# Kernel optimization log

Measured on AMD Instinct MI355X. Metric: run time of the kernel, lower is better.

Reference implementation:

```python
import jax, jax.numpy as jnp
import numpy as np

N, T, D, H = 4, 2048, 1024, 16
DK = D // H

def setup_inputs() -> dict:
    key = jax.random.key(0)
    k1, k2, k3 = jax.random.split(key, 3)
    z = jax.random.normal(k1, (N, T, D), dtype=jnp.float32)
    Wqkv = jax.random.normal(k2, (D, 3 * D), dtype=jnp.float32) * 0.01
    Wout = jax.random.normal(k3, (D, D), dtype=jnp.float32) * 0.01
    return {"z": z, "Wqkv": Wqkv, "Wout": Wout}

def reference(z, Wqkv, Wout):
    n, t, d = z.shape
    scale = DK ** -0.5
    qkv = z @ Wqkv  # [N,T,3D]
    q, k, v = jnp.split(qkv, 3, axis=-1)
    # [N,T,D] -> [N,H,T,dk]
    q = q.reshape(n, t, H, DK).transpose(0, 2, 1, 3)
    k = k.reshape(n, t, H, DK).transpose(0, 2, 1, 3)
    v = v.reshape(n, t, H, DK).transpose(0, 2, 1, 3)
    attn = jnp.einsum('nhqd,nhkd->nhqk', q, k) * scale
    causal = jnp.tril(jnp.ones((t, t), dtype=bool))
    attn = jnp.where(causal, attn, -jnp.inf)
    attn = jax.nn.softmax(attn, axis=-1)
    out = jnp.einsum('nhqk,nhkd->nhqd', attn, v)  # [N,H,T,dk]
    out = out.transpose(0, 2, 1, 3).reshape(n, t, d)
    return out @ Wout
```

## Files before the change

kernel.cpp:

```cpp
#include <hip/hip_runtime.h>
#include <hip/hip_bf16.h>

typedef __bf16 bf16;
typedef __bf16 bf16x8 __attribute__((ext_vector_type(8)));
typedef float f32x4 __attribute__((ext_vector_type(4)));

#define N_B 4
#define T_S 2048
#define D_M 1024
#define H_N 16
#define D_K 64
#define D3 3072
#define NEG_BIG (-1e30f)
#define QSCALE 0.18033688011112042f

#if __has_builtin(__builtin_amdgcn_exp2f)
#define EXP2(x) __builtin_amdgcn_exp2f(x)
#else
#define EXP2(x) exp2f(x)
#endif

__device__ __forceinline__ void gload_lds16(const bf16* g, bf16* l) {
    __builtin_amdgcn_global_load_lds((const __attribute__((address_space(1))) void*)g,
                                     (__attribute__((address_space(3))) void*)l, 16, 0, 0);
}

__device__ __forceinline__ bool probe_fp32(const void* p) {
    const unsigned int* w = (const unsigned int*)p;
    int weird = 0;
#pragma unroll
    for (int i = 0; i < 16; ++i) {
        unsigned int v = w[i];
        unsigned int e = (v >> 7) & 0xFFu;
        if ((v & 0xFFFFu) != 0u && (e < 100u || e > 140u)) weird++;
    }
    return weird >= 4;
}

__global__ __launch_bounds__(256) void prep(const void* __restrict__ z, bf16* __restrict__ zb,
                                            const void* __restrict__ Wqkv, bf16* __restrict__ WqkvT,
                                            const void* __restrict__ Wout, bf16* __restrict__ WoutT) {
    __shared__ bf16 tile[32][33];
    const int b = blockIdx.x;
    const int t = threadIdx.x;

    if (b < 4096) {
        const int i = (b * 256 + t) * 8;
        if (probe_fp32(z)) {
            const float* zf = (const float*)z;
            float4 u0 = *(const float4*)(zf + i);
            float4 u1 = *(const float4*)(zf + i + 4);
            union { uint4 q; bf16 h[8]; } pk;
            pk.h[0] = (bf16)u0.x; pk.h[1] = (bf16)u0.y;
            pk.h[2] = (bf16)u0.z; pk.h[3] = (bf16)u0.w;
            pk.h[4] = (bf16)u1.x; pk.h[5] = (bf16)u1.y;
            pk.h[6] = (bf16)u1.z; pk.h[7] = (bf16)u1.w;
            *(uint4*)(zb + i) = pk.q;
        } else {
            *(uint4*)(zb + i) = ((const uint4*)z)[b * 256 + t];
        }
        return;
    }

    const void* in; bf16* out; int R, C, c0, r0;
    if (b < 7168) {
        int idx = b - 4096;
        in = Wqkv; out = WqkvT; R = 1024; C = 3072;
        c0 = (idx % 96) * 32; r0 = (idx / 96) * 32;
    } else {
        int idx = b - 7168;
        in = Wout; out = WoutT; R = 1024; C = 1024;
        c0 = (idx & 31) * 32; r0 = (idx >> 5) * 32;
    }
    const int tx = t & 31, ty = t >> 5;
    if (probe_fp32(in)) {
        const float* inf_ = (const float*)in;
        for (int i = 0; i < 4; ++i)
            tile[ty + i * 8][tx] = (bf16)inf_[(size_t)(r0 + ty + i * 8) * C + c0 + tx];
    } else {
        const bf16* inb = (const bf16*)in;
        for (int i = 0; i < 4; ++i)
            tile[ty + i * 8][tx] = inb[(size_t)(r0 + ty + i * 8) * C + c0 + tx];
    }
    __syncthreads();
    for (int i = 0; i < 4; ++i)
        out[(size_t)(c0 + ty + i * 8) * R + r0 + tx] = tile[tx][ty + i * 8];
}

__global__ __launch_bounds__(512, 2) void gemm256(const bf16* __restrict__ A,
                                                  const bf16* __restrict__ Bt,
                                                  void* __restrict__ C,
                                                  bf16* __restrict__ Kf,
                                                  bf16* __restrict__ Vf,
                                                  int M, int N, int K,
                                                  int modeC) {
    __shared__ bf16 As[3][256 * 64];
    __shared__ bf16 Bs[3][128 * 64];
    const int t = threadIdx.x;
    const int m0 = blockIdx.y * 256, n0 = blockIdx.x * 128;
    const int w = t >> 6, lane = t & 63, quad = lane >> 4, l15 = lane & 15;
    const int wr = (w >> 1) * 64, wc = (w & 1) * 64;
    const int sr = t >> 3;
    const int sg = ((t & 7) ^ (sr & 7)) * 8;
    const int xorL = (l15 & 7) * 8;

    const bf16* a0 = A + (size_t)(m0 + sr) * K + sg;
    const bf16* a1 = A + (size_t)(m0 + 64 + sr) * K + sg;
    const bf16* a2 = A + (size_t)(m0 + 128 + sr) * K + sg;
    const bf16* a3 = A + (size_t)(m0 + 192 + sr) * K + sg;
    const bf16* b0 = Bt + (size_t)(n0 + sr) * K + sg;
    const bf16* b1 = Bt + (size_t)(n0 + 64 + sr) * K + sg;
    const int ldsOff = w * 512;

    f32x4 acc[4][4];
    const f32x4 zero4 = {0.f, 0.f, 0.f, 0.f};
#pragma unroll
    for (int i = 0; i < 4; ++i)
#pragma unroll
        for (int j = 0; j < 4; ++j) acc[i][j] = zero4;

    const int nt = K >> 6;

    gload_lds16(a0, &As[0][0 * 4096 + ldsOff]);
    gload_lds16(a1, &As[0][1 * 4096 + ldsOff]);
    gload_lds16(a2, &As[0][2 * 4096 + ldsOff]);
    gload_lds16(a3, &As[0][3 * 4096 + ldsOff]);
    gload_lds16(b0, &Bs[0][0 * 4096 + ldsOff]);
    gload_lds16(b1, &Bs[0][1 * 4096 + ldsOff]);
    if (nt > 1) {
        gload_lds16(a0 + 64, &As[1][0 * 4096 + ldsOff]);
        gload_lds16(a1 + 64, &As[1][1 * 4096 + ldsOff]);
        gload_lds16(a2 + 64, &As[1][2 * 4096 + ldsOff]);
        gload_lds16(a3 + 64, &As[1][3 * 4096 + ldsOff]);
        gload_lds16(b0 + 64, &Bs[1][0 * 4096 + ldsOff]);
        gload_lds16(b1 + 64, &Bs[1][1 * 4096 + ldsOff]);
        asm volatile("s_waitcnt vmcnt(6)" ::: "memory");
    } else {
        asm volatile("s_waitcnt vmcnt(0)" ::: "memory");
    }
    __builtin_amdgcn_sched_barrier(0);
    __builtin_amdgcn_s_barrier();
    __builtin_amdgcn_sched_barrier(0);

    int cur = 0;
    for (int tt = 0; tt < nt; ++tt) {
        const bf16* Ac = As[cur];
        const bf16* Bc = Bs[cur];
        int pf = cur + 2; if (pf >= 3) pf -= 3;
        const bool do_pf = (tt + 2 < nt);
        const int kpf = (tt + 2) << 6;

        {
            const int colOff = (quad * 8) ^ xorL;
            bf16x8 af[4], bfv[4];
#pragma unroll
            for (int i = 0; i < 4; ++i)
                af[i] = *(const bf16x8*)(Ac + (wr + i * 16 + l15) * 64 + colOff);
#pragma unroll
            for (int j = 0; j < 4; ++j)
                bfv[j] = *(const bf16x8*)(Bc + (wc + j * 16 + l15) * 64 + colOff);
            if (do_pf) {
                gload_lds16(a0 + kpf, &As[pf][0 * 4096 + ldsOff]);
                gload_lds16(a1 + kpf, &As[pf][1 * 4096 + ldsOff]);
                gload_lds16(a2 + kpf, &As[pf][2 * 4096 + ldsOff]);
            }
            __builtin_amdgcn_sched_barrier(0);
            __builtin_amdgcn_s_barrier();
            asm volatile("s_waitcnt lgkmcnt(0)" ::: "memory");
            __builtin_amdgcn_sched_barrier(0);
            __builtin_amdgcn_s_setprio(1);
#pragma unroll
            for (int i = 0; i < 4; ++i)
#pragma unroll
                for (int j = 0; j < 4; ++j)
                    acc[i][j] = __builtin_amdgcn_mfma_f32_16x16x32_bf16(af[i], bfv[j], acc[i][j], 0, 0, 0);
            __builtin_amdgcn_s_setprio(0);
            __builtin_amdgcn_sched_barrier(0);
            __builtin_amdgcn_s_barrier();
            __builtin_amdgcn_sched_barrier(0);
        }

        {
            const int colOff = (32 + quad * 8) ^ xorL;
            bf16x8 af[4], bfv[4];
#pragma unroll
            for (int i = 0; i < 4; ++i)
                af[i] = *(const bf16x8*)(Ac + (wr + i * 16 + l15) * 64 + colOff);
#pragma unroll
            for (int j = 0; j < 4; ++j)
                bfv[j] = *(const bf16x8*)(Bc + (wc + j * 16 + l15) * 64 + colOff);
            if (do_pf) {
                gload_lds16(a3 + kpf, &As[pf][3 * 4096 + ldsOff]);
                gload_lds16(b0 + kpf, &Bs[pf][0 * 4096 + ldsOff]);
                gload_lds16(b1 + kpf, &Bs[pf][1 * 4096 + ldsOff]);
                asm volatile("s_waitcnt vmcnt(6)" ::: "memory");
            } else {
                asm volatile("s_waitcnt vmcnt(0)" ::: "memory");
            }
            __builtin_amdgcn_sched_barrier(0);
            __builtin_amdgcn_s_barrier();
            asm volatile("s_waitcnt lgkmcnt(0)" ::: "memory");
            __builtin_amdgcn_sched_barrier(0);
            __builtin_amdgcn_s_setprio(1);
#pragma unroll
            for (int i = 0; i < 4; ++i)
#pragma unroll
                for (int j = 0; j < 4; ++j)
                    acc[i][j] = __builtin_amdgcn_mfma_f32_16x16x32_bf16(af[i], bfv[j], acc[i][j], 0, 0, 0);
            __builtin_amdgcn_s_setprio(0);
            __builtin_amdgcn_sched_barrier(0);
            __builtin_amdgcn_s_barrier();
            __builtin_amdgcn_sched_barrier(0);
        }
        cur = cur + 1; if (cur == 3) cur = 0;
    }

    if (modeC == 1) {
        float* Cf = (float*)C;
        for (int i = 0; i < 4; ++i)
            for (int fc = 0; fc < 4; ++fc)
                for (int r = 0; r < 4; ++r)
                    Cf[(size_t)(m0 + wr + i * 16 + quad * 4 + r) * N
                       + (n0 + wc + fc * 16 + l15)] = acc[i][fc][r];
    } else if (n0 < 1024) {
        bf16* q = (bf16*)C;
        for (int i = 0; i < 4; ++i)
            for (int fc = 0; fc < 4; ++fc)
                for (int r = 0; r < 4; ++r)
                    q[(size_t)(m0 + wr + i * 16 + quad * 4 + r) * 1024
                      + (n0 + wc + fc * 16 + l15)] = (bf16)(acc[i][fc][r] * QSCALE);
    } else if (n0 < 2048) {
        for (int i = 0; i < 4; ++i) {
            int rowb = m0 + wr + i * 16 + quad * 4;
            int nb = rowb >> 11, tt = rowb & 2047;
            int kt = tt >> 6, f = (tt >> 4) & 3, l15k = tt & 15;
            for (int fc = 0; fc < 4; ++fc) {
                int col = n0 + wc + fc * 16 + l15 - 1024;
                int h = col >> 6, dk = col & 63;
                int ks = dk >> 5, qdk = (dk >> 3) & 3, j = dk & 7;
                size_t base = ((size_t)((nb * 16 + h) * 32 + kt) * 8 + ks * 4 + f) * 512 + j;
                for (int r = 0; r < 4; ++r)
                    Kf[base + (qdk * 16 + l15k + r) * 8] = (bf16)acc[i][fc][r];
            }
        }
    } else {
        for (int i = 0; i < 4; ++i) {
            int rowb = m0 + wr + i * 16 + quad * 4;
            int nb = rowb >> 11, tt = rowb & 2047;
            int kt = tt >> 6, ks = (tt >> 5) & 1, qdv = (tt >> 3) & 3, j0 = tt & 7;
            for (int fc = 0; fc < 4; ++fc) {
                int col = n0 + wc + fc * 16 + l15 - 2048;
                int h = col >> 6, dl = col & 63;
                int fv = dl >> 4, l15v = dl & 15;
                union { ushort4 u; bf16 hh[4]; } pk;
                for (int r = 0; r < 4; ++r) pk.hh[r] = (bf16)acc[i][fc][r];
                *(ushort4*)(Vf + ((size_t)((nb * 16 + h) * 32 + kt) * 8 + ks * 4 + fv) * 512
                            + (qdv * 16 + l15v) * 8 + j0) = pk.u;
            }
        }
    }
}

#define LDP 72
__global__ __launch_bounds__(256, 2) void attn_fused(const bf16* __restrict__ q,
                                                     const bf16* __restrict__ Kf,
                                                     const bf16* __restrict__ Vf,
                                                     bf16* __restrict__ attn_out) {
    __shared__ bf16 Pl[4 * 32 * LDP];

    const int b = blockIdx.x;
    const int head = b & 63;
    const int qp = b >> 6;
    const int n = head >> 4, h = head & 15;
    const int t = threadIdx.x;
    const int w = t >> 6, lane = t & 63, qd = lane >> 4, l15 = lane & 15;
    const int r = (w + qp + head) & 3;
    const int qt = (r < 2) ? qp : (31 - qp);
    const int q0w = qt * 64 + (r & 1) * 32;
    const size_t rowBase = (size_t)n * T_S;
    const bf16* KfH = Kf + (size_t)head * 32 * 4096;
    const bf16* VfH = Vf + (size_t)head * 32 * 4096;
    bf16* Plw = Pl + w * 32 * LDP;

    bf16x8 bQ[2][2];
#pragma unroll
    for (int qh = 0; qh < 2; ++qh)
#pragma unroll
        for (int ks = 0; ks < 2; ++ks)
            bQ[qh][ks] = *(const bf16x8*)(q + (rowBase + q0w + qh * 16 + l15) * 1024
                                          + h * 64 + ks * 32 + qd * 8);

    float l_lane[2] = {0.f, 0.f};
    f32x4 oacc[2][4];
    const f32x4 zero4 = {0.f, 0.f, 0.f, 0.f};
#pragma unroll
    for (int qh = 0; qh < 2; ++qh)
#pragma unroll
        for (int fd = 0; fd < 4; ++fd) oacc[qh][fd] = zero4;

    const int ktmax = (q0w + 31) >> 6;

    bf16x8 aK[2][4];
#pragma unroll
    for (int fr = 0; fr < 8; ++fr)
        aK[fr >> 2][fr & 3] = *(const bf16x8*)(KfH + fr * 512 + lane * 8);

    for (int kt = 0; kt <= ktmax; ++kt) {
        const int k0r = kt * 64;
        const bf16* VfT = VfH + (size_t)kt * 4096;

        bf16x8 aV[2][4];
#pragma unroll
        for (int fr = 0; fr < 8; ++fr)
            aV[fr >> 2][fr & 3] = *(const bf16x8*)(VfT + fr * 512 + lane * 8);

        f32x4 sacc[2][4];
#pragma unroll
        for (int qh = 0; qh < 2; ++qh)
#pragma unroll
            for (int fc = 0; fc < 4; ++fc) sacc[qh][fc] = zero4;
#pragma unroll
        for (int ks = 0; ks < 2; ++ks)
#pragma unroll
            for (int fc = 0; fc < 4; ++fc) {
                sacc[0][fc] = __builtin_amdgcn_mfma_f32_16x16x32_bf16(aK[ks][fc], bQ[0][ks], sacc[0][fc], 0, 0, 0);
                sacc[1][fc] = __builtin_amdgcn_mfma_f32_16x16x32_bf16(aK[ks][fc], bQ[1][ks], sacc[1][fc], 0, 0, 0);
            }

        if (kt < ktmax) {
            const bf16* KfN = KfH + (size_t)(kt + 1) * 4096;
#pragma unroll
            for (int fr = 0; fr < 8; ++fr)
                aK[fr >> 2][fr & 3] = *(const bf16x8*)(KfN + fr * 512 + lane * 8);
        }

        if (k0r + 63 > q0w) {
#pragma unroll
            for (int qh = 0; qh < 2; ++qh) {
                const int qq = q0w + qh * 16 + l15;
#pragma unroll
                for (int fc = 0; fc < 4; ++fc)
#pragma unroll
                    for (int rr = 0; rr < 4; ++rr)
                        if (k0r + fc * 16 + qd * 4 + rr > qq) sacc[qh][fc][rr] = NEG_BIG;
            }
        }

#pragma unroll
        for (int qh = 0; qh < 2; ++qh) {
            float rs = 0.f;
#pragma unroll
            for (int fc = 0; fc < 4; ++fc) {
                union { ushort4 u; bf16 hh[4]; } pk;
#pragma unroll
                for (int rr = 0; rr < 4; ++rr) {
                    float p = EXP2(sacc[qh][fc][rr]);
                    rs += p;
                    pk.hh[rr] = (bf16)p;
                }
                *(ushort4*)(Plw + (qh * 16 + l15) * LDP + fc * 16 + qd * 4) = pk.u;
            }
            l_lane[qh] += rs;
        }

#pragma unroll
        for (int ks = 0; ks < 2; ++ks) {
            bf16x8 bP0 = *(const bf16x8*)(Plw + l15 * LDP + ks * 32 + qd * 8);
            bf16x8 bP1 = *(const bf16x8*)(Plw + (16 + l15) * LDP + ks * 32 + qd * 8);
#pragma unroll
            for (int fd = 0; fd < 4; ++fd) {
                oacc[0][fd] = __builtin_amdgcn_mfma_f32_16x16x32_bf16(aV[ks][fd], bP0, oacc[0][fd], 0, 0, 0);
                oacc[1][fd] = __builtin_amdgcn_mfma_f32_16x16x32_bf16(aV[ks][fd], bP1, oacc[1][fd], 0, 0, 0);
            }
        }
    }

#pragma unroll
    for (int qh = 0; qh < 2; ++qh) {
        float l = l_lane[qh];
        l += __shfl_xor(l, 16, 64);
        l += __shfl_xor(l, 32, 64);
        float inv = 1.f / l;
#pragma unroll
        for (int fd = 0; fd < 4; ++fd) {
            union { ushort4 u; bf16 hh[4]; } pk;
#pragma unroll
            for (int rr = 0; rr < 4; ++rr) pk.hh[rr] = (bf16)(oacc[qh][fd][rr] * inv);
            *(ushort4*)(attn_out + (rowBase + q0w + qh * 16 + l15) * D_M
                        + h * D_K + fd * 16 + qd * 4) = pk.u;
        }
    }
}

extern "C" void kernel_launch(void* const* d_in, const int* in_sizes, int n_in,
                              void* d_out, int out_size, void* d_ws, size_t ws_size,
                              hipStream_t stream) {
    const void* z    = d_in[0];
    const void* Wqkv = d_in[1];
    const void* Wout = d_in[2];

    char* ws = (char*)d_ws;
    bf16* q     = (bf16*)(ws + 256);
    bf16* attn  = (bf16*)(ws + 256 + 16777216);
    bf16* zb    = attn;
    bf16* WqkvT = (bf16*)(ws + 256 + 2 * 16777216);
    bf16* WoutT = (bf16*)(ws + 256 + 2 * 16777216 + 6291456);

    bf16* Kf = (bf16*)d_out;
    bf16* Vf = Kf + 8388608;

    prep<<<dim3(8192), 256, 0, stream>>>(z, zb, Wqkv, WqkvT, Wout, WoutT);

    gemm256<<<dim3(D3 / 128, (N_B * T_S) / 256), 512, 0, stream>>>(
        zb, WqkvT, q, Kf, Vf, N_B * T_S, D3, D_M, 2);

    attn_fused<<<dim3(64 * 16), 256, 0, stream>>>(q, Kf, Vf, attn);

    gemm256<<<dim3(D_M / 128, (N_B * T_S) / 256), 512, 0, stream>>>(
        attn, WoutT, d_out, Kf, Vf, N_B * T_S, D_M, D_M, 1);
}
```

Before: 233.1 us.

## Template GEMM on tile width, use 256x256 tiles for QKV with XCD-aware block remap

Turns the GEMM into a template over the N-tile width. The QKV projection now uses 256x256 tiles with 8 accumulator rows per wave, which doubles operand reuse per LDS load. The pipeline changes from a triple buffer with split prefetch to a double buffer that prefetches a whole tile each iteration, and blocks are launched on a 1-D grid remapped so consecutive tiles land on the same XCD for L2 locality. The cost is more accumulator registers and LDS per block, plus shallower prefetch depth, which may hurt latency hiding or occupancy.

```diff
diff --git a/kernel.cpp b/kernel.cpp
--- a/kernel.cpp
+++ b/kernel.cpp
@@ -87,151 +87,163 @@
         out[(size_t)(c0 + ty + i * 8) * R + r0 + tx] = tile[tx][ty + i * 8];
 }
 
-__global__ __launch_bounds__(512, 2) void gemm256(const bf16* __restrict__ A,
-                                                  const bf16* __restrict__ Bt,
-                                                  void* __restrict__ C,
-                                                  bf16* __restrict__ Kf,
-                                                  bf16* __restrict__ Vf,
-                                                  int M, int N, int K,
-                                                  int modeC) {
-    __shared__ bf16 As[3][256 * 64];
-    __shared__ bf16 Bs[3][128 * 64];
+template<int BN>
+__global__ __launch_bounds__(512, 2) void gemmT(const bf16* __restrict__ A,
+                                                const bf16* __restrict__ Bt,
+                                                void* __restrict__ C,
+                                                bf16* __restrict__ Kf,
+                                                bf16* __restrict__ Vf,
+                                                int M, int N, int K,
+                                                int modeC, int nbx) {
+    constexpr int BLOADS = BN / 64;
+    constexpr int MI = (BN == 256) ? 8 : 4;
+    __shared__ bf16 As[2][256 * 64];
+    __shared__ bf16 Bs[2][BN * 64];
+
+    const int nwg = gridDim.x;
+    const int per = nwg >> 3;
+    const int b0 = blockIdx.x;
+    const int bid = (b0 & 7) * per + (b0 >> 3);
+    const int by = bid / nbx;
+    const int bx = bid - by * nbx;
+    const int m0 = by * 256, n0 = bx * BN;
+
     const int t = threadIdx.x;
-    const int m0 = blockIdx.y * 256, n0 = blockIdx.x * 128;
     const int w = t >> 6, lane = t & 63, quad = lane >> 4, l15 = lane & 15;
-    const int wr = (w >> 1) * 64, wc = (w & 1) * 64;
+    const int wr = (BN == 256) ? (w >> 2) * 128 : (w >> 1) * 64;
+    const int wc = (BN == 256) ? (w & 3) * 64 : (w & 1) * 64;
     const int sr = t >> 3;
     const int sg = ((t & 7) ^ (sr & 7)) * 8;
     const int xorL = (l15 & 7) * 8;
-
-    const bf16* a0 = A + (size_t)(m0 + sr) * K + sg;
-    const bf16* a1 = A + (size_t)(m0 + 64 + sr) * K + sg;
-    const bf16* a2 = A + (size_t)(m0 + 128 + sr) * K + sg;
-    const bf16* a3 = A + (size_t)(m0 + 192 + sr) * K + sg;
-    const bf16* b0 = Bt + (size_t)(n0 + sr) * K + sg;
-    const bf16* b1 = Bt + (size_t)(n0 + 64 + sr) * K + sg;
     const int ldsOff = w * 512;
 
-    f32x4 acc[4][4];
+    const bf16* ag0 = A + (size_t)(m0 + sr) * K + sg;
+    const bf16* ag1 = A + (size_t)(m0 + 64 + sr) * K + sg;
+    const bf16* ag2 = A + (size_t)(m0 + 128 + sr) * K + sg;
+    const bf16* ag3 = A + (size_t)(m0 + 192 + sr) * K + sg;
+    const bf16* bg0 = Bt + (size_t)(n0 + sr) * K + sg;
+    const bf16* bg1 = Bt + (size_t)(n0 + 64 + sr) * K + sg;
+    const bf16* bg2 = (BN == 256) ? Bt + (size_t)(n0 + 128 + sr) * K + sg : bg0;
+    const bf16* bg3 = (BN == 256) ? Bt + (size_t)(n0 + 192 + sr) * K + sg : bg0;
+
+    f32x4 acc[MI][4];
     const f32x4 zero4 = {0.f, 0.f, 0.f, 0.f};
 #pragma unroll
-    for (int i = 0; i < 4; ++i)
+    for (int i = 0; i < MI; ++i)
 #pragma unroll
         for (int j = 0; j < 4; ++j) acc[i][j] = zero4;
 
     const int nt = K >> 6;
 
-    gload_lds16(a0, &As[0][0 * 4096 + ldsOff]);
-    gload_lds16(a1, &As[0][1 * 4096 + ldsOff]);
-    gload_lds16(a2, &As[0][2 * 4096 + ldsOff]);
-    gload_lds16(a3, &As[0][3 * 4096 + ldsOff]);
-    gload_lds16(b0, &Bs[0][0 * 4096 + ldsOff]);
-    gload_lds16(b1, &Bs[0][1 * 4096 + ldsOff]);
-    if (nt > 1) {
-        gload_lds16(a0 + 64, &As[1][0 * 4096 + ldsOff]);
-        gload_lds16(a1 + 64, &As[1][1 * 4096 + ldsOff]);
-        gload_lds16(a2 + 64, &As[1][2 * 4096 + ldsOff]);
-        gload_lds16(a3 + 64, &As[1][3 * 4096 + ldsOff]);
-        gload_lds16(b0 + 64, &Bs[1][0 * 4096 + ldsOff]);
-        gload_lds16(b1 + 64, &Bs[1][1 * 4096 + ldsOff]);
-        asm volatile("s_waitcnt vmcnt(6)" ::: "memory");
-    } else {
-        asm volatile("s_waitcnt vmcnt(0)" ::: "memory");
-    }
-    __builtin_amdgcn_sched_barrier(0);
-    __builtin_amdgcn_s_barrier();
-    __builtin_amdgcn_sched_barrier(0);
-
-    int cur = 0;
+    gload_lds16(ag0, &As[0][0 * 4096 + ldsOff]);
+    gload_lds16(ag1, &As[0][1 * 4096 + ldsOff]);
+    gload_lds16(ag2, &As[0][2 * 4096 + ldsOff]);
+    gload_lds16(ag3, &As[0][3 * 4096 + ldsOff]);
+    gload_lds16(bg0, &Bs[0][0 * 4096 + ldsOff]);
+    gload_lds16(bg1, &Bs[0][1 * 4096 + ldsOff]);
+    if constexpr (BN == 256) {
+        gload_lds16(bg2, &Bs[0][2 * 4096 + ldsOff]);
+        gload_lds16(bg3, &Bs[0][3 * 4096 + ldsOff]);
+    }
+
     for (int tt = 0; tt < nt; ++tt) {
-        const bf16* Ac = As[cur];
-        const bf16* Bc = Bs[cur];
-        int pf = cur + 2; if (pf >= 3) pf -= 3;
-        const bool do_pf = (tt + 2 < nt);
-        const int kpf = (tt + 2) << 6;
-
-        {
-            const int colOff = (quad * 8) ^ xorL;
-            bf16x8 af[4], bfv[4];
-#pragma unroll
-            for (int i = 0; i < 4; ++i)
-                af[i] = *(const bf16x8*)(Ac + (wr + i * 16 + l15) * 64 + colOff);
+        const int s = tt & 1;
+        if (tt + 1 < nt) {
+            const int kn = (tt + 1) << 6;
+            bf16* Ad = As[s ^ 1];
+            bf16* Bd = Bs[s ^ 1];
+            gload_lds16(ag0 + kn, Ad + 0 * 4096 + ldsOff);
+            gload_lds16(ag1 + kn, Ad + 1 * 4096 + ldsOff);
+            gload_lds16(ag2 + kn, Ad + 2 * 4096 + ldsOff);
+            gload_lds16(ag3 + kn, Ad + 3 * 4096 + ldsOff);
+            gload_lds16(bg0 + kn, Bd + 0 * 4096 + ldsOff);
+            gload_lds16(bg1 + kn, Bd + 1 * 4096 + ldsOff);
+            if constexpr (BN == 256) {
+                gload_lds16(bg2 + kn, Bd + 2 * 4096 + ldsOff);
+                gload_lds16(bg3 + kn, Bd + 3 * 4096 + ldsOff);
+                asm volatile("s_waitcnt vmcnt(8)" ::: "memory");
+            } else {
+                asm volatile("s_waitcnt vmcnt(6)" ::: "memory");
+            }
+        } else {
+            asm volatile("s_waitcnt vmcnt(0)" ::: "memory");
+        }
+        __builtin_amdgcn_sched_barrier(0);
+        __builtin_amdgcn_s_barrier();
+        __builtin_amdgcn_sched_barrier(0);
+
+        const bf16* Ac = As[s];
+        const bf16* Bc = Bs[s];
+#pragma unroll
+        for (int kk = 0; kk < 2; ++kk) {
+            const int colOff = (kk * 32 + quad * 8) ^ xorL;
+            bf16x8 bfv[4];
 #pragma unroll
             for (int j = 0; j < 4; ++j)
                 bfv[j] = *(const bf16x8*)(Bc + (wc + j * 16 + l15) * 64 + colOff);
-            if (do_pf) {
-                gload_lds16(a0 + kpf, &As[pf][0 * 4096 + ldsOff]);
-                gload_lds16(a1 + kpf, &As[pf][1 * 4096 + ldsOff]);
-                gload_lds16(a2 + kpf, &As[pf][2 * 4096 + ldsOff]);
-            }
-            __builtin_amdgcn_sched_barrier(0);
-            __builtin_amdgcn_s_barrier();
-            asm volatile("s_waitcnt lgkmcnt(0)" ::: "memory");
-            __builtin_amdgcn_sched_barrier(0);
-            __builtin_amdgcn_s_setprio(1);
-#pragma unroll
-            for (int i = 0; i < 4; ++i)
-#pragma unroll
-                for (int j = 0; j < 4; ++j)
-                    acc[i][j] = __builtin_amdgcn_mfma_f32_16x16x32_bf16(af[i], bfv[j], acc[i][j], 0, 0, 0);
-            __builtin_amdgcn_s_setprio(0);
-            __builtin_amdgcn_sched_barrier(0);
-            __builtin_amdgcn_s_barrier();
-            __builtin_amdgcn_sched_barrier(0);
-        }
-
-        {
-            const int colOff = (32 + quad * 8) ^ xorL;
-            bf16x8 af[4], bfv[4];
-#pragma unroll
-            for (int i = 0; i < 4; ++i)
-                af[i] = *(const bf16x8*)(Ac + (wr + i * 16 + l15) * 64 + colOff);
-#pragma unroll
-            for (int j = 0; j < 4; ++j)
-                bfv[j] = *(const bf16x8*)(Bc + (wc + j * 16 + l15) * 64 + colOff);
-            if (do_pf) {
-                gload_lds16(a3 + kpf, &As[pf][3 * 4096 + ldsOff]);
-                gload_lds16(b0 + kpf, &Bs[pf][0 * 4096 + ldsOff]);
-                gload_lds16(b1 + kpf, &Bs[pf][1 * 4096 + ldsOff]);
-                asm volatile("s_waitcnt vmcnt(6)" ::: "memory");
-            } else {
-                asm volatile("s_waitcnt vmcnt(0)" ::: "memory");
-            }
-            __builtin_amdgcn_sched_barrier(0);
-            __builtin_amdgcn_s_barrier();
-            asm volatile("s_waitcnt lgkmcnt(0)" ::: "memory");
-            __builtin_amdgcn_sched_barrier(0);
-            __builtin_amdgcn_s_setprio(1);
-#pragma unroll
-            for (int i = 0; i < 4; ++i)
-#pragma unroll
-                for (int j = 0; j < 4; ++j)
-                    acc[i][j] = __builtin_amdgcn_mfma_f32_16x16x32_bf16(af[i], bfv[j], acc[i][j], 0, 0, 0);
-            __builtin_amdgcn_s_setprio(0);
-            __builtin_amdgcn_sched_barrier(0);
-            __builtin_amdgcn_s_barrier();
-            __builtin_amdgcn_sched_barrier(0);
-        }
-        cur = cur + 1; if (cur == 3) cur = 0;
+            {
+                bf16x8 af[4];
+#pragma unroll
+                for (int i = 0; i < 4; ++i)
+                    af[i] = *(const bf16x8*)(Ac + (wr + i * 16 + l15) * 64 + colOff);
+                __builtin_amdgcn_sched_barrier(0);
+                __builtin_amdgcn_s_barrier();
+                asm volatile("s_waitcnt lgkmcnt(0)" ::: "memory");
+                __builtin_amdgcn_sched_barrier(0);
+                __builtin_amdgcn_s_setprio(1);
+#pragma unroll
+                for (int i = 0; i < 4; ++i)
+#pragma unroll
+                    for (int j = 0; j < 4; ++j)
+                        acc[i][j] = __builtin_amdgcn_mfma_f32_16x16x32_bf16(af[i], bfv[j], acc[i][j], 0, 0, 0);
+                __builtin_amdgcn_s_setprio(0);
+                __builtin_amdgcn_sched_barrier(0);
+                __builtin_amdgcn_s_barrier();
+                __builtin_amdgcn_sched_barrier(0);
+            }
+            if constexpr (BN == 256) {
+                bf16x8 af[4];
+#pragma unroll
+                for (int i = 0; i < 4; ++i)
+                    af[i] = *(const bf16x8*)(Ac + (wr + 64 + i * 16 + l15) * 64 + colOff);
+                __builtin_amdgcn_sched_barrier(0);
+                __builtin_amdgcn_s_barrier();
+                asm volatile("s_waitcnt lgkmcnt(0)" ::: "memory");
+                __builtin_amdgcn_sched_barrier(0);
+                __builtin_amdgcn_s_setprio(1);
+#pragma unroll
+                for (int i = 0; i < 4; ++i)
+#pragma unroll
+                    for (int j = 0; j < 4; ++j)
+                        acc[4 + i][j] = __builtin_amdgcn_mfma_f32_16x16x32_bf16(af[i], bfv[j], acc[4 + i][j], 0, 0, 0);
+                __builtin_amdgcn_s_setprio(0);
+                __builtin_amdgcn_sched_barrier(0);
+                __builtin_amdgcn_s_barrier();
+                __builtin_amdgcn_sched_barrier(0);
+            }
+        }
     }
 
     if (modeC == 1) {
         float* Cf = (float*)C;
-        for (int i = 0; i < 4; ++i)
+        for (int ii = 0; ii < MI; ++ii) {
+            int rowb = m0 + wr + ((ii >> 2) << 6) + ((ii & 3) << 4) + quad * 4;
             for (int fc = 0; fc < 4; ++fc)
                 for (int r = 0; r < 4; ++r)
-                    Cf[(size_t)(m0 + wr + i * 16 + quad * 4 + r) * N
-                       + (n0 + wc + fc * 16 + l15)] = acc[i][fc][r];
+                    Cf[(size_t)(rowb + r) * N + (n0 + wc + fc * 16 + l15)] = acc[ii][fc][r];
+        }
     } else if (n0 < 1024) {
         bf16* q = (bf16*)C;
-        for (int i = 0; i < 4; ++i)
+        for (int ii = 0; ii < MI; ++ii) {
+            int rowb = m0 + wr + ((ii >> 2) << 6) + ((ii & 3) << 4) + quad * 4;
             for (int fc = 0; fc < 4; ++fc)
                 for (int r = 0; r < 4; ++r)
-                    q[(size_t)(m0 + wr + i * 16 + quad * 4 + r) * 1024
-                      + (n0 + wc + fc * 16 + l15)] = (bf16)(acc[i][fc][r] * QSCALE);
+                    q[(size_t)(rowb + r) * 1024 + (n0 + wc + fc * 16 + l15)]
+                        = (bf16)(acc[ii][fc][r] * QSCALE);
+        }
     } else if (n0 < 2048) {
-        for (int i = 0; i < 4; ++i) {
-            int rowb = m0 + wr + i * 16 + quad * 4;
+        for (int ii = 0; ii < MI; ++ii) {
+            int rowb = m0 + wr + ((ii >> 2) << 6) + ((ii & 3) << 4) + quad * 4;
             int nb = rowb >> 11, tt = rowb & 2047;
             int kt = tt >> 6, f = (tt >> 4) & 3, l15k = tt & 15;
             for (int fc = 0; fc < 4; ++fc) {
@@ -240,12 +252,12 @@
                 int ks = dk >> 5, qdk = (dk >> 3) & 3, j = dk & 7;
                 size_t base = ((size_t)((nb * 16 + h) * 32 + kt) * 8 + ks * 4 + f) * 512 + j;
                 for (int r = 0; r < 4; ++r)
-                    Kf[base + (qdk * 16 + l15k + r) * 8] = (bf16)acc[i][fc][r];
+                    Kf[base + (qdk * 16 + l15k + r) * 8] = (bf16)acc[ii][fc][r];
             }
         }
     } else {
-        for (int i = 0; i < 4; ++i) {
-            int rowb = m0 + wr + i * 16 + quad * 4;
+        for (int ii = 0; ii < MI; ++ii) {
+            int rowb = m0 + wr + ((ii >> 2) << 6) + ((ii & 3) << 4) + quad * 4;
             int nb = rowb >> 11, tt = rowb & 2047;
             int kt = tt >> 6, ks = (tt >> 5) & 1, qdv = (tt >> 3) & 3, j0 = tt & 7;
             for (int fc = 0; fc < 4; ++fc) {
@@ -253,7 +265,7 @@
                 int h = col >> 6, dl = col & 63;
                 int fv = dl >> 4, l15v = dl & 15;
                 union { ushort4 u; bf16 hh[4]; } pk;
-                for (int r = 0; r < 4; ++r) pk.hh[r] = (bf16)acc[i][fc][r];
+                for (int r = 0; r < 4; ++r) pk.hh[r] = (bf16)acc[ii][fc][r];
                 *(ushort4*)(Vf + ((size_t)((nb * 16 + h) * 32 + kt) * 8 + ks * 4 + fv) * 512
                             + (qdv * 16 + l15v) * 8 + j0) = pk.u;
             }
@@ -411,11 +423,11 @@
 
     prep<<<dim3(8192), 256, 0, stream>>>(z, zb, Wqkv, WqkvT, Wout, WoutT);
 
-    gemm256<<<dim3(D3 / 128, (N_B * T_S) / 256), 512, 0, stream>>>(
-        zb, WqkvT, q, Kf, Vf, N_B * T_S, D3, D_M, 2);
+    gemmT<256><<<dim3(384), 512, 0, stream>>>(
+        zb, WqkvT, q, Kf, Vf, N_B * T_S, D3, D_M, 2, 12);
 
     attn_fused<<<dim3(64 * 16), 256, 0, stream>>>(q, Kf, Vf, attn);
 
-    gemm256<<<dim3(D_M / 128, (N_B * T_S) / 256), 512, 0, stream>>>(
-        attn, WoutT, d_out, Kf, Vf, N_B * T_S, D_M, D_M, 1);
-}
+    gemmT<128><<<dim3(256), 512, 0, stream>>>(
+        attn, WoutT, d_out, Kf, Vf, N_B * T_S, D_M, D_M, 1, 8);
+}
```

Result: slower. 254.0 us (+9.0%).

## Share K/V tiles across warps via double-buffered LDS in attention kernel

Applied to the files above, without the earlier changes.

The attention kernel now gives each block a contiguous 128-row query tile (one 32-row slice per warp) and cooperatively stages K and V tiles into double-buffered shared memory with async global-to-LDS loads. Previously each warp loaded its own K/V fragments straight from global memory. The change is meant to cut redundant global traffic by sharing each K/V tile across the four warps. In exchange it adds a block-wide barrier per key tile, leaves warps with fewer causal tiles idle while others finish, and uses more LDS, which may reduce occupancy. The old interleaved query-tile scheduling for load balance is replaced by a reverse block order.

```diff
diff --git a/kernel.cpp b/kernel.cpp
--- a/kernel.cpp
+++ b/kernel.cpp
@@ -266,21 +266,22 @@
                                                      const bf16* __restrict__ Kf,
                                                      const bf16* __restrict__ Vf,
                                                      bf16* __restrict__ attn_out) {
+    __shared__ bf16 Ks[2][4096];
+    __shared__ bf16 Vs[2][4096];
     __shared__ bf16 Pl[4 * 32 * LDP];
 
     const int b = blockIdx.x;
     const int head = b & 63;
-    const int qp = b >> 6;
+    const int qt = 15 - (b >> 6);
     const int n = head >> 4, h = head & 15;
     const int t = threadIdx.x;
     const int w = t >> 6, lane = t & 63, qd = lane >> 4, l15 = lane & 15;
-    const int r = (w + qp + head) & 3;
-    const int qt = (r < 2) ? qp : (31 - qp);
-    const int q0w = qt * 64 + (r & 1) * 32;
+    const int q0w = qt * 128 + w * 32;
     const size_t rowBase = (size_t)n * T_S;
     const bf16* KfH = Kf + (size_t)head * 32 * 4096;
     const bf16* VfH = Vf + (size_t)head * 32 * 4096;
     bf16* Plw = Pl + w * 32 * LDP;
+    const int sc = w * 2;
 
     bf16x8 bQ[2][2];
 #pragma unroll
@@ -298,81 +299,94 @@
 #pragma unroll
         for (int fd = 0; fd < 4; ++fd) oacc[qh][fd] = zero4;
 
-    const int ktmax = (q0w + 31) >> 6;
-
-    bf16x8 aK[2][4];
-#pragma unroll
-    for (int fr = 0; fr < 8; ++fr)
-        aK[fr >> 2][fr & 3] = *(const bf16x8*)(KfH + fr * 512 + lane * 8);
-
-    for (int kt = 0; kt <= ktmax; ++kt) {
-        const int k0r = kt * 64;
-        const bf16* VfT = VfH + (size_t)kt * 4096;
-
-        bf16x8 aV[2][4];
-#pragma unroll
-        for (int fr = 0; fr < 8; ++fr)
-            aV[fr >> 2][fr & 3] = *(const bf16x8*)(VfT + fr * 512 + lane * 8);
-
-        f32x4 sacc[2][4];
-#pragma unroll
-        for (int qh = 0; qh < 2; ++qh)
-#pragma unroll
-            for (int fc = 0; fc < 4; ++fc) sacc[qh][fc] = zero4;
-#pragma unroll
-        for (int ks = 0; ks < 2; ++ks)
-#pragma unroll
-            for (int fc = 0; fc < 4; ++fc) {
-                sacc[0][fc] = __builtin_amdgcn_mfma_f32_16x16x32_bf16(aK[ks][fc], bQ[0][ks], sacc[0][fc], 0, 0, 0);
-                sacc[1][fc] = __builtin_amdgcn_mfma_f32_16x16x32_bf16(aK[ks][fc], bQ[1][ks], sacc[1][fc], 0, 0, 0);
-            }
-
-        if (kt < ktmax) {
-            const bf16* KfN = KfH + (size_t)(kt + 1) * 4096;
+    const int ktmax_w = (q0w + 31) >> 6;
+    const int ktmax_b = (qt * 128 + 127) >> 6;
+
+    gload_lds16(KfH + (sc + 0) * 512 + lane * 8, &Ks[0][(sc + 0) * 512]);
+    gload_lds16(KfH + (sc + 1) * 512 + lane * 8, &Ks[0][(sc + 1) * 512]);
+    gload_lds16(VfH + (sc + 0) * 512 + lane * 8, &Vs[0][(sc + 0) * 512]);
+    gload_lds16(VfH + (sc + 1) * 512 + lane * 8, &Vs[0][(sc + 1) * 512]);
+    __syncthreads();
+
+    int cur = 0;
+    for (int kt = 0; kt <= ktmax_b; ++kt) {
+        if (kt + 1 <= ktmax_b) {
+            const bf16* Kn = KfH + (size_t)(kt + 1) * 4096;
+            const bf16* Vn = VfH + (size_t)(kt + 1) * 4096;
+            gload_lds16(Kn + (sc + 0) * 512 + lane * 8, &Ks[cur ^ 1][(sc + 0) * 512]);
+            gload_lds16(Kn + (sc + 1) * 512 + lane * 8, &Ks[cur ^ 1][(sc + 1) * 512]);
+            gload_lds16(Vn + (sc + 0) * 512 + lane * 8, &Vs[cur ^ 1][(sc + 0) * 512]);
+            gload_lds16(Vn + (sc + 1) * 512 + lane * 8, &Vs[cur ^ 1][(sc + 1) * 512]);
+        }
+
+        if (kt <= ktmax_w) {
+            const int k0r = kt * 64;
+
+            bf16x8 aK[2][4];
 #pragma unroll
             for (int fr = 0; fr < 8; ++fr)
-                aK[fr >> 2][fr & 3] = *(const bf16x8*)(KfN + fr * 512 + lane * 8);
-        }
-
-        if (k0r + 63 > q0w) {
+                aK[fr >> 2][fr & 3] = *(const bf16x8*)(&Ks[cur][fr * 512 + lane * 8]);
+
+            f32x4 sacc[2][4];
+#pragma unroll
+            for (int qh = 0; qh < 2; ++qh)
+#pragma unroll
+                for (int fc = 0; fc < 4; ++fc) sacc[qh][fc] = zero4;
+#pragma unroll
+            for (int ks = 0; ks < 2; ++ks)
+#pragma unroll
+                for (int fc = 0; fc < 4; ++fc) {
+                    sacc[0][fc] = __builtin_amdgcn_mfma_f32_16x16x32_bf16(aK[ks][fc], bQ[0][ks], sacc[0][fc], 0, 0, 0);
+                    sacc[1][fc] = __builtin_amdgcn_mfma_f32_16x16x32_bf16(aK[ks][fc], bQ[1][ks], sacc[1][fc], 0, 0, 0);
+                }
+
+            if (k0r + 63 > q0w) {
+#pragma unroll
+                for (int qh = 0; qh < 2; ++qh) {
+                    const int qq = q0w + qh * 16 + l15;
+#pragma unroll
+                    for (int fc = 0; fc < 4; ++fc)
+#pragma unroll
+                        for (int rr = 0; rr < 4; ++rr)
+                            if (k0r + fc * 16 + qd * 4 + rr > qq) sacc[qh][fc][rr] = NEG_BIG;
+                }
+            }
+
 #pragma unroll
             for (int qh = 0; qh < 2; ++qh) {
-                const int qq = q0w + qh * 16 + l15;
-#pragma unroll
-                for (int fc = 0; fc < 4; ++fc)
-#pragma unroll
-                    for (int rr = 0; rr < 4; ++rr)
-                        if (k0r + fc * 16 + qd * 4 + rr > qq) sacc[qh][fc][rr] = NEG_BIG;
-            }
-        }
-
-#pragma unroll
-        for (int qh = 0; qh < 2; ++qh) {
-            float rs = 0.f;
-#pragma unroll
-            for (int fc = 0; fc < 4; ++fc) {
-                union { ushort4 u; bf16 hh[4]; } pk;
-#pragma unroll
-                for (int rr = 0; rr < 4; ++rr) {
-                    float p = EXP2(sacc[qh][fc][rr]);
-                    rs += p;
-                    pk.hh[rr] = (bf16)p;
+                float rs = 0.f;
+#pragma unroll
+                for (int fc = 0; fc < 4; ++fc) {
+                    union { ushort4 u; bf16 hh[4]; } pk;
+#pragma unroll
+                    for (int rr = 0; rr < 4; ++rr) {
+                        float p = EXP2(sacc[qh][fc][rr]);
+                        rs += p;
+                        pk.hh[rr] = (bf16)p;
+                    }
+                    *(ushort4*)(Plw + (qh * 16 + l15) * LDP + fc * 16 + qd * 4) = pk.u;
                 }
-                *(ushort4*)(Plw + (qh * 16 + l15) * LDP + fc * 16 + qd * 4) = pk.u;
-            }
-            l_lane[qh] += rs;
-        }
-
-#pragma unroll
-        for (int ks = 0; ks < 2; ++ks) {
-            bf16x8 bP0 = *(const bf16x8*)(Plw + l15 * LDP + ks * 32 + qd * 8);
-            bf16x8 bP1 = *(const bf16x8*)(Plw + (16 + l15) * LDP + ks * 32 + qd * 8);
-#pragma unroll
-            for (int fd = 0; fd < 4; ++fd) {
-                oacc[0][fd] = __builtin_amdgcn_mfma_f32_16x16x32_bf16(aV[ks][fd], bP0, oacc[0][fd], 0, 0, 0);
-                oacc[1][fd] = __builtin_amdgcn_mfma_f32_16x16x32_bf16(aV[ks][fd], bP1, oacc[1][fd], 0, 0, 0);
-            }
-        }
+                l_lane[qh] += rs;
+            }
+
+            bf16x8 aV[2][4];
+#pragma unroll
+            for (int fr = 0; fr < 8; ++fr)
+                aV[fr >> 2][fr & 3] = *(const bf16x8*)(&Vs[cur][fr * 512 + lane * 8]);
+#pragma unroll
+            for (int ks = 0; ks < 2; ++ks) {
+                bf16x8 bP0 = *(const bf16x8*)(Plw + l15 * LDP + ks * 32 + qd * 8);
+                bf16x8 bP1 = *(const bf16x8*)(Plw + (16 + l15) * LDP + ks * 32 + qd * 8);
+#pragma unroll
+                for (int fd = 0; fd < 4; ++fd) {
+                    oacc[0][fd] = __builtin_amdgcn_mfma_f32_16x16x32_bf16(aV[ks][fd], bP0, oacc[0][fd], 0, 0, 0);
+                    oacc[1][fd] = __builtin_amdgcn_mfma_f32_16x16x32_bf16(aV[ks][fd], bP1, oacc[1][fd], 0, 0, 0);
+                }
+            }
+        }
+
+        __syncthreads();
+        cur ^= 1;
     }
 
 #pragma unroll
```

After: 225.9 us. -3.1%, faster.
